# Kernel tuning notes

Hardware: AMD Instinct MI355X
Metric: run time of the kernel (lower is better)

The kernel has to match this reference:

```python
import jax, jax.numpy as jnp
import numpy as np

T, N, DEG = 8, 8192, 15
H = 4


def _gat(x, src, dst, wl, wr, a, b):
    """GATv2Conv with concat=False (heads averaged). x: [N, Cin] -> [N, Cout].
    e_ij = a_h . LeakyReLU(Wl x_j + Wr x_i); softmax over incoming edges of i;
    messages are Wl x_j (PyG GATv2 convention, self-loops already in edge list)."""
    n = x.shape[0]
    h, c = a.shape
    gl = (x @ wl).reshape(n, h, c)  # source-side transform
    gr = (x @ wr).reshape(n, h, c)  # target-side transform
    z = jax.nn.leaky_relu(gl[src] + gr[dst], 0.2)          # [E,H,C]
    e = jnp.einsum('ehc,hc->eh', z, a)                     # [E,H]
    m = jax.ops.segment_max(e, dst, num_segments=n)        # [N,H]
    ex = jnp.exp(e - m[dst])
    den = jax.ops.segment_sum(ex, dst, num_segments=n)     # [N,H]
    msg = jax.ops.segment_sum(ex[:, :, None] * gl[src], dst, num_segments=n)
    return (msg / den[:, :, None]).mean(axis=1) + b


def _d3(x, esrc, edst, wl, wr, a, b):
    # spatio-temporal graph conv: GATv2 applied independently per timestep
    return jax.lax.map(lambda args: _gat(args[0], args[1], args[2], wl, wr, a, b),
                       (x, esrc, edst))


def setup_inputs() -> dict:
    key = jax.random.key(0)
    ks = iter(jax.random.split(key, 32))
    x = jax.random.normal(next(ks), (T, N, 64), dtype=jnp.float32)
    # fixed-degree random graph per timestep + self loops (PyG add_self_loops=True)
    dst_base = jnp.repeat(jnp.arange(N, dtype=jnp.int32), DEG)
    src_r = jax.random.randint(next(ks), (T, N * DEG), 0, N, dtype=jnp.int32)
    loop = jnp.arange(N, dtype=jnp.int32)
    edge_src = jnp.concatenate([src_r, jnp.broadcast_to(loop, (T, N))], axis=1)
    edge_dst = jnp.concatenate([jnp.broadcast_to(dst_base, (T, N * DEG)),
                                jnp.broadcast_to(loop, (T, N))], axis=1)

    def gat_p(k, cin, cout):
        k1, k2, k3 = jax.random.split(k, 3)
        s = 1.0 / np.sqrt(cin)
        return ((jax.random.normal(k1, (cin, H * cout)) * s).astype(jnp.float32),
                (jax.random.normal(k2, (cin, H * cout)) * s).astype(jnp.float32),
                (jax.random.normal(k3, (H, cout)) * s).astype(jnp.float32),
                jnp.zeros((cout,), jnp.float32))

    inp = {"x": x, "edge_src": edge_src, "edge_dst": edge_dst}
    for name, cin, cout in [("c1", 64, 128), ("c2", 128, 64), ("c3", 64, 64), ("c4", 128, 64),
                            ("r11", 64, 64), ("r12", 64, 64), ("r2", 128, 128),
                            ("f11", 64, 64), ("f2", 128, 128)]:
        wl, wr, a, b = gat_p(next(ks), cin, cout)
        inp[name + "_wl"], inp[name + "_wr"], inp[name + "_a"], inp[name + "_b"] = wl, wr, a, b
    # ConvTranspose1d(k=1) == per-node linear conv_ch -> in_channels; then Linear in_channels -> original_dim
    for name, cin, cout in [("r3", 128, 64), ("f3", 128, 64), ("r4", 64, 64), ("f4", 64, 64)]:
        inp[name + "_w"] = (jax.random.normal(next(ks), (cin, cout)) * (1.0 / np.sqrt(cin))).astype(jnp.float32)
        inp[name + "_b"] = jnp.zeros((cout,), jnp.float32)
    return inp


def reference(x, edge_src, edge_dst,
              c1_wl, c1_wr, c1_a, c1_b, c2_wl, c2_wr, c2_a, c2_b,
              c3_wl, c3_wr, c3_a, c3_b, c4_wl, c4_wr, c4_a, c4_b,
              r11_wl, r11_wr, r11_a, r11_b, r12_wl, r12_wr, r12_a, r12_b,
              r2_wl, r2_wr, r2_a, r2_b, r3_w, r3_b, r4_w, r4_b,
              f11_wl, f11_wr, f11_a, f11_b, f2_wl, f2_wr, f2_a, f2_b,
              f3_w, f3_b, f4_w, f4_b):
    elu = jax.nn.elu
    out = elu(_d3(x, edge_src, edge_dst, c1_wl, c1_wr, c1_a, c1_b))           # [T,N,128]
    emb = elu(_d3(out, edge_src, edge_dst, c2_wl, c2_wr, c2_a, c2_b))         # [T,N,64]
    emb = elu(jnp.concatenate([_d3(emb, edge_src, edge_dst, c3_wl, c3_wr, c3_a, c3_b), emb], -1))  # [T,N,128]
    emb = elu(_d3(emb, edge_src, edge_dst, c4_wl, c4_wr, c4_a, c4_b))         # [T,N,64]

    # reconstruction branch on edges at t = -1
    s1, d1 = edge_src[-1], edge_dst[-1]
    r = elu(_gat(emb[-1], s1, d1, r11_wl, r11_wr, r11_a, r11_b))
    r = elu(jnp.concatenate([_gat(r, s1, d1, r12_wl, r12_wr, r12_a, r12_b), r], -1))  # [N,128]
    # F.dropout in eval mode -> identity
    r = elu(_gat(r, s1, d1, r2_wl, r2_wr, r2_a, r2_b))
    r = jnp.tanh(r @ r3_w + r3_b)
    recon = r @ r4_w + r4_b

    # forecasting branch on edges at t = -2 (original reuses reconstruct12 here)
    s2, d2 = edge_src[-2], edge_dst[-2]
    f = elu(_gat(emb[-2], s2, d2, f11_wl, f11_wr, f11_a, f11_b))
    f = elu(jnp.concatenate([_gat(f, s2, d2, r12_wl, r12_wr, r12_a, r12_b), f], -1))
    f = elu(_gat(f, s2, d2, f2_wl, f2_wr, f2_a, f2_b))
    f = jnp.tanh(f @ f3_w + f3_b)
    forecast = f @ f4_w + f4_b
    return (recon, forecast, emb)
```

## Files before the change

### kernel.cpp

```cpp
#include <hip/hip_runtime.h>
#include <cmath>

constexpr int T_   = 8;
constexpr int N_   = 8192;
constexpr int DEG_ = 15;
constexpr int E_   = N_ * (DEG_ + 1);
constexpr float L2E_ = 1.44269504f;

__device__ __forceinline__ float elu1(float v) { return v > 0.f ? v : expm1f(v); }

typedef __attribute__((ext_vector_type(8))) short bf16x8;
typedef __attribute__((ext_vector_type(4))) float f32x4;

__device__ __forceinline__ ushort f2bf(float x) {
  uint u = __float_as_uint(x);
  return (ushort)((u + 0x7FFFu + ((u >> 16) & 1u)) >> 16);
}
__device__ __forceinline__ float bf2f(ushort h) {
  return __uint_as_float(((uint)h) << 16);
}

template<int CTRL>
__device__ __forceinline__ float dpp_add(float x) {
  const int t = __builtin_amdgcn_mov_dpp(__float_as_int(x), CTRL, 0xf, 0xf, true);
  return x + __int_as_float(t);
}
__device__ __forceinline__ float row_reduce16(float x) {
  x = dpp_add<0x121>(x);
  x = dpp_add<0x122>(x);
  x = dpp_add<0x124>(x);
  x = dpp_add<0x128>(x);
  return x;
}

__global__ __launch_bounds__(256) void split_x(
    const float* __restrict__ X, ushort* __restrict__ XH, ushort* __restrict__ XL, int n4)
{
  const int i = blockIdx.x * 256 + threadIdx.x;
  if (i >= n4) return;
  const float4 v = ((const float4*)X)[i];
  const ushort h0 = f2bf(v.x), h1 = f2bf(v.y), h2 = f2bf(v.z), h3 = f2bf(v.w);
  ushort4 hh; hh.x = h0; hh.y = h1; hh.z = h2; hh.w = h3;
  ushort4 ll;
  ll.x = f2bf(v.x - bf2f(h0)); ll.y = f2bf(v.y - bf2f(h1));
  ll.z = f2bf(v.z - bf2f(h2)); ll.w = f2bf(v.w - bf2f(h3));
  ((ushort4*)XH)[i] = hh;
  ((ushort4*)XL)[i] = ll;
}

__global__ __launch_bounds__(256) void split_wt(
    const float* __restrict__ Wl, const float* __restrict__ Wr,
    ushort* __restrict__ WH, ushort* __restrict__ WL, int K, int HC)
{
  const int idx = blockIdx.x * 256 + threadIdx.x;
  if (idx >= 2 * HC * K) return;
  const int k = idx % K;
  const int n = (idx / K) % HC;
  const int s = idx / (K * HC);
  const float v = (s ? Wr : Wl)[k * HC + n];
  const ushort h = f2bf(v);
  WH[idx] = h;
  WL[idx] = f2bf(v - bf2f(h));
}

__global__ __launch_bounds__(256) void gemm_mfma(
    const ushort* __restrict__ Ah, const ushort* __restrict__ Al,
    const ushort* __restrict__ Wh, const ushort* __restrict__ Wl,
    float* __restrict__ Cl, float* __restrict__ Cr,
    int M, int Ncol, int K, int nt)
{
  __shared__ alignas(16) ushort lAh[4 * 1032];
  __shared__ alignas(16) ushort lAl[4 * 1032];
  __shared__ alignas(16) ushort lBh[4 * 520];
  __shared__ alignas(16) ushort lBl[4 * 520];

  const int z = blockIdx.z;
  const int t = (z < nt) ? z : z - nt;
  const int side = (z < nt) ? 0 : 1;
  const ushort* __restrict__ Bh = Wh + (size_t)side * Ncol * K;
  const ushort* __restrict__ Bl = Wl + (size_t)side * Ncol * K;
  float* __restrict__ C = (side ? Cr : Cl) + (size_t)t * M * Ncol;
  const size_t aoff = (size_t)t * M * K;

  const int bm = blockIdx.x * 128, bn = blockIdx.y * 64;
  const int tid = threadIdx.x;
  const int wid = tid >> 6, lane = tid & 63;
  const int l15 = lane & 15, lk = lane >> 4;

  f32x4 acc[2][4] = {};

  for (int k0 = 0; k0 < K; k0 += 32) {
    #pragma unroll
    for (int c = 0; c < 2; c++) {
      const int ch = tid + c * 256;
      const int row = ch >> 2, kc = ch & 3;
      const size_t ga = aoff + (size_t)(bm + row) * K + (k0 + kc * 8);
      *(uint4*)&lAh[kc * 1032 + row * 8] = *(const uint4*)(Ah + ga);
      *(uint4*)&lAl[kc * 1032 + row * 8] = *(const uint4*)(Al + ga);
    }
    {
      const int col = tid >> 2, kc = tid & 3;
      const size_t gb = (size_t)(bn + col) * K + (k0 + kc * 8);
      *(uint4*)&lBh[kc * 520 + col * 8] = *(const uint4*)(Bh + gb);
      *(uint4*)&lBl[kc * 520 + col * 8] = *(const uint4*)(Bl + gb);
    }
    __syncthreads();

    bf16x8 ah[2], al[2], bh4[4], bl4[4];
    const int r0 = wid * 32;
    #pragma unroll
    for (int rf = 0; rf < 2; rf++) {
      const int ro = (r0 + rf * 16 + l15) * 8;
      ah[rf] = *(const bf16x8*)&lAh[lk * 1032 + ro];
      al[rf] = *(const bf16x8*)&lAl[lk * 1032 + ro];
    }
    #pragma unroll
    for (int cf = 0; cf < 4; cf++) {
      const int co = (cf * 16 + l15) * 8;
      bh4[cf] = *(const bf16x8*)&lBh[lk * 520 + co];
      bl4[cf] = *(const bf16x8*)&lBl[lk * 520 + co];
    }
    #pragma unroll
    for (int rf = 0; rf < 2; rf++)
      #pragma unroll
      for (int cf = 0; cf < 4; cf++) {
        acc[rf][cf] = __builtin_amdgcn_mfma_f32_16x16x32_bf16(ah[rf], bh4[cf], acc[rf][cf], 0, 0, 0);
        acc[rf][cf] = __builtin_amdgcn_mfma_f32_16x16x32_bf16(ah[rf], bl4[cf], acc[rf][cf], 0, 0, 0);
        acc[rf][cf] = __builtin_amdgcn_mfma_f32_16x16x32_bf16(al[rf], bh4[cf], acc[rf][cf], 0, 0, 0);
      }
    __syncthreads();
  }

  #pragma unroll
  for (int rf = 0; rf < 2; rf++)
    #pragma unroll
    for (int cf = 0; cf < 4; cf++) {
      const int col = bn + cf * 16 + l15;
      #pragma unroll
      for (int reg = 0; reg < 4; reg++) {
        const int row = bm + wid * 32 + rf * 16 + lk * 4 + reg;
        C[(size_t)row * Ncol + col] = acc[rf][cf][reg];
      }
    }
}

template<int EPI>
__global__ __launch_bounds__(256) void gemm_k(
    const float* __restrict__ A, const float* __restrict__ B,
    float* __restrict__ C, const float* __restrict__ bias,
    int M, int Ncol, int K)
{
  __shared__ float As[16][68];
  __shared__ float Bs[16][64];

  const int tid = threadIdx.x;
  const int tx = tid & 15, ty = tid >> 4;
  const int bm = blockIdx.x * 64, bn = blockIdx.y * 64;

  const int arow = tid >> 2;
  const int akc  = (tid & 3) * 4;
  const int brow = tid >> 4;
  const int bc4  = (tid & 15) * 4;

  float acc[4][4];
  #pragma unroll
  for (int i = 0; i < 4; i++)
    #pragma unroll
    for (int j = 0; j < 4; j++) acc[i][j] = 0.f;

  for (int k0 = 0; k0 < K; k0 += 16) {
    const float4 va = *(const float4*)(A + (size_t)(bm + arow) * K + (k0 + akc));
    const float4 vb = *(const float4*)(B + (size_t)(k0 + brow) * Ncol + (bn + bc4));
    As[akc + 0][arow] = va.x; As[akc + 1][arow] = va.y;
    As[akc + 2][arow] = va.z; As[akc + 3][arow] = va.w;
    *(float4*)&Bs[brow][bc4] = vb;
    __syncthreads();
    #pragma unroll
    for (int kk = 0; kk < 16; kk++) {
      const float4 av = *(const float4*)&As[kk][ty * 4];
      const float4 bv = *(const float4*)&Bs[kk][tx * 4];
      const float a4[4] = {av.x, av.y, av.z, av.w};
      const float b4[4] = {bv.x, bv.y, bv.z, bv.w};
      #pragma unroll
      for (int i = 0; i < 4; i++)
        #pragma unroll
        for (int j = 0; j < 4; j++)
          acc[i][j] = fmaf(a4[i], b4[j], acc[i][j]);
    }
    __syncthreads();
  }

  #pragma unroll
  for (int i = 0; i < 4; i++) {
    const int row = bm + ty * 4 + i;
    const int col = bn + tx * 4;
    float v[4] = {acc[i][0], acc[i][1], acc[i][2], acc[i][3]};
    #pragma unroll
    for (int j = 0; j < 4; j++) v[j] += bias[col + j];
    if (EPI == 1) {
      #pragma unroll
      for (int j = 0; j < 4; j++) v[j] = tanhf(v[j]);
    }
    *(float4*)(C + (size_t)row * Ncol + col) = make_float4(v[0], v[1], v[2], v[3]);
  }
}

template<bool CONCAT>
__global__ __launch_bounds__(256) void gat_agg256(
    const float* __restrict__ GL, const float* __restrict__ GR,
    const float* __restrict__ aw_, const float* __restrict__ bias,
    const int* __restrict__ esrc, float* __restrict__ out,
    const float* __restrict__ csrc,
    ushort* __restrict__ SHo, ushort* __restrict__ SLo, int numNodes)
{
  constexpr int HC = 256, C = 64;
  constexpr int OSTR = CONCAT ? 128 : 64;

  const int lane = threadIdx.x & 63;
  const int wid  = threadIdx.x >> 6;
  const int gid  = blockIdx.x * 4 + wid;
  if (gid >= numNodes) return;
  const int t = gid >> 13;
  const int i = gid & (N_ - 1);

  const float* __restrict__ gl = GL + (size_t)t * N_ * HC;
  const int*   __restrict__ es = esrc + (size_t)t * E_ + (size_t)i * DEG_;

  float gr[4], a6[4], a4c[4];
  {
    const float4 gv = *(const float4*)(GR + (size_t)gid * HC + lane * 4);
    const float4 av = *(const float4*)(aw_ + lane * 4);
    gr[0] = gv.x; gr[1] = gv.y; gr[2] = gv.z; gr[3] = gv.w;
    a6[0] = 0.6f * L2E_ * av.x; a6[1] = 0.6f * L2E_ * av.y;
    a6[2] = 0.6f * L2E_ * av.z; a6[3] = 0.6f * L2E_ * av.w;
    a4c[0] = 0.4f * L2E_ * av.x; a4c[1] = 0.4f * L2E_ * av.y;
    a4c[2] = 0.4f * L2E_ * av.z; a4c[3] = 0.4f * L2E_ * av.w;
  }

  float acc[4] = {0.f, 0.f, 0.f, 0.f};
  float den = 0.f, m = -1e30f;

  #pragma unroll
  for (int b = 0; b < 4; b++) {
    int js[4];
    #pragma unroll
    for (int q = 0; q < 4; q++) {
      const int ek = b * 4 + q;
      js[q] = (ek < DEG_) ? es[ek] : i;
    }
    float g[4][4];
    #pragma unroll
    for (int q = 0; q < 4; q++) {
      const float4 v = *(const float4*)(gl + (size_t)js[q] * HC + lane * 4);
      g[q][0] = v.x; g[q][1] = v.y; g[q][2] = v.z; g[q][3] = v.w;
    }
    float p[4];
    #pragma unroll
    for (int q = 0; q < 4; q++) {
      float s = 0.f;
      #pragma unroll
      for (int u = 0; u < 4; u++) {
        const float z = g[q][u] + gr[u];
        s = fmaf(z, a6[u], s);
        s = fmaf(fabsf(z), a4c[u], s);
      }
      p[q] = s;
    }
    #pragma unroll
    for (int q = 0; q < 4; q++) p[q] = row_reduce16(p[q]);

    const float bmax = fmaxf(fmaxf(p[0], p[1]), fmaxf(p[2], p[3]));
    const float nm   = fmaxf(m, bmax);
    const float sc   = exp2f(m - nm);
    den *= sc;
    #pragma unroll
    for (int u = 0; u < 4; u++) acc[u] *= sc;
    #pragma unroll
    for (int q = 0; q < 4; q++) {
      const float w = exp2f(p[q] - nm);
      den += w;
      #pragma unroll
      for (int u = 0; u < 4; u++) acc[u] = fmaf(w, g[q][u], acc[u]);
    }
    m = nm;
  }

  const float inv = 0.25f / den;
  #pragma unroll
  for (int u = 0; u < 4; u++) acc[u] *= inv;
  #pragma unroll
  for (int u = 0; u < 4; u++) {
    acc[u] += __shfl_xor(acc[u], 16);
    acc[u] += __shfl_xor(acc[u], 32);
  }

  float* orow = out + (size_t)gid * OSTR;
  if (lane < 16) {
    float o[4];
    #pragma unroll
    for (int u = 0; u < 4; u++)
      o[u] = elu1(acc[u] + bias[lane * 4 + u]);
    *(float4*)(orow + lane * 4) = make_float4(o[0], o[1], o[2], o[3]);
    if (SHo) {
      ushort4 hh, ll;
      hh.x = f2bf(o[0]); hh.y = f2bf(o[1]); hh.z = f2bf(o[2]); hh.w = f2bf(o[3]);
      ll.x = f2bf(o[0] - bf2f(hh.x)); ll.y = f2bf(o[1] - bf2f(hh.y));
      ll.z = f2bf(o[2] - bf2f(hh.z)); ll.w = f2bf(o[3] - bf2f(hh.w));
      *(ushort4*)(SHo + (size_t)gid * OSTR + lane * 4) = hh;
      *(ushort4*)(SLo + (size_t)gid * OSTR + lane * 4) = ll;
    }
  } else if (CONCAT && lane < 32) {
    const int q = lane - 16;
    const float4 v = *(const float4*)(csrc + (size_t)gid * C + q * 4);
    const float o0 = elu1(v.x), o1 = elu1(v.y), o2 = elu1(v.z), o3 = elu1(v.w);
    *(float4*)(orow + C + q * 4) = make_float4(o0, o1, o2, o3);
    if (SHo) {
      ushort4 hh, ll;
      hh.x = f2bf(o0); hh.y = f2bf(o1); hh.z = f2bf(o2); hh.w = f2bf(o3);
      ll.x = f2bf(o0 - bf2f(hh.x)); ll.y = f2bf(o1 - bf2f(hh.y));
      ll.z = f2bf(o2 - bf2f(hh.z)); ll.w = f2bf(o3 - bf2f(hh.w));
      *(ushort4*)(SHo + (size_t)gid * OSTR + C + q * 4) = hh;
      *(ushort4*)(SLo + (size_t)gid * OSTR + C + q * 4) = ll;
    }
  }
}

__global__ __launch_bounds__(256) void gat_agg512(
    const float* __restrict__ GL, const float* __restrict__ GR,
    const float* __restrict__ aw_, const float* __restrict__ bias,
    const int* __restrict__ esrc, float* __restrict__ out)
{
  __shared__ float smem[4][128];

  const int lane = threadIdx.x & 63;
  const int h    = threadIdx.x >> 6;
  const int gid  = blockIdx.x;
  const int t = gid >> 13;
  const int i = gid & (N_ - 1);

  const float* __restrict__ gl = GL + (size_t)t * N_ * 512;
  const int*   __restrict__ es = esrc + (size_t)t * E_ + (size_t)i * DEG_;
  const int cb = h * 128 + lane * 2;

  float gr0, gr1, a60, a61, a40, a41;
  {
    const float2 gv = *(const float2*)(GR + (size_t)gid * 512 + cb);
    const float2 av = *(const float2*)(aw_ + cb);
    gr0 = gv.x; gr1 = gv.y;
    a60 = 0.6f * L2E_ * av.x; a61 = 0.6f * L2E_ * av.y;
    a40 = 0.4f * L2E_ * av.x; a41 = 0.4f * L2E_ * av.y;
  }

  float acc0 = 0.f, acc1 = 0.f, den = 0.f, m = -1e30f;

  #pragma unroll
  for (int b = 0; b < 4; b++) {
    int js[4];
    #pragma unroll
    for (int q = 0; q < 4; q++) {
      const int ek = b * 4 + q;
      js[q] = (ek < DEG_) ? es[ek] : i;
    }
    float g[4][2];
    #pragma unroll
    for (int q = 0; q < 4; q++) {
      const float2 v = *(const float2*)(gl + (size_t)js[q] * 512 + cb);
      g[q][0] = v.x; g[q][1] = v.y;
    }
    float p[4];
    #pragma unroll
    for (int q = 0; q < 4; q++) {
      const float z0 = g[q][0] + gr0;
      const float z1 = g[q][1] + gr1;
      float s = z0 * a60;
      s = fmaf(fabsf(z0), a40, s);
      s = fmaf(z1, a61, s);
      s = fmaf(fabsf(z1), a41, s);
      p[q] = s;
    }
    #pragma unroll
    for (int q = 0; q < 4; q++) {
      p[q] = row_reduce16(p[q]);
      p[q] += __shfl_xor(p[q], 16);
      p[q] += __shfl_xor(p[q], 32);
    }
    const float bmax = fmaxf(fmaxf(p[0], p[1]), fmaxf(p[2], p[3]));
    const float nm   = fmaxf(m, bmax);
    const float sc   = exp2f(m - nm);
    den *= sc; acc0 *= sc; acc1 *= sc;
    #pragma unroll
    for (int q = 0; q < 4; q++) {
      const float w = exp2f(p[q] - nm);
      den += w;
      acc0 = fmaf(w, g[q][0], acc0);
      acc1 = fmaf(w, g[q][1], acc1);
    }
    m = nm;
  }

  const float inv = 0.25f / den;
  smem[h][lane * 2]     = acc0 * inv;
  smem[h][lane * 2 + 1] = acc1 * inv;
  __syncthreads();

  if (h == 0) {
    const int c = lane * 2;
    float s0 = smem[0][c] + smem[1][c] + smem[2][c] + smem[3][c];
    float s1 = smem[0][c + 1] + smem[1][c + 1] + smem[2][c + 1] + smem[3][c + 1];
    s0 = elu1(s0 + bias[c]);
    s1 = elu1(s1 + bias[c + 1]);
    *(float2*)(out + (size_t)gid * 128 + c) = make_float2(s0, s1);
  }
}

extern "C" void kernel_launch(void* const* d_in, const int* in_sizes, int n_in,
                              void* d_out, int out_size, void* d_ws, size_t ws_size,
                              hipStream_t stream)
{
  (void)in_sizes; (void)n_in; (void)out_size; (void)ws_size;

  const float* x  = (const float*)d_in[0];
  const int*   es = (const int*)d_in[1];
  const float *c1_wl=(const float*)d_in[3], *c1_wr=(const float*)d_in[4], *c1_a=(const float*)d_in[5], *c1_b=(const float*)d_in[6];
  const float *c2_wl=(const float*)d_in[7], *c2_wr=(const float*)d_in[8], *c2_a=(const float*)d_in[9], *c2_b=(const float*)d_in[10];
  const float *c3_wl=(const float*)d_in[11],*c3_wr=(const float*)d_in[12],*c3_a=(const float*)d_in[13],*c3_b=(const float*)d_in[14];
  const float *c4_wl=(const float*)d_in[15],*c4_wr=(const float*)d_in[16],*c4_a=(const float*)d_in[17],*c4_b=(const float*)d_in[18];
  const float *r11_wl=(const float*)d_in[19],*r11_wr=(const float*)d_in[20],*r11_a=(const float*)d_in[21],*r11_b=(const float*)d_in[22];
  const float *r12_wl=(const float*)d_in[23],*r12_wr=(const float*)d_in[24],*r12_a=(const float*)d_in[25],*r12_b=(const float*)d_in[26];
  const float *r2_wl=(const float*)d_in[27],*r2_wr=(const float*)d_in[28],*r2_a=(const float*)d_in[29],*r2_b=(const float*)d_in[30];
  const float *f11_wl=(const float*)d_in[31],*f11_wr=(const float*)d_in[32],*f11_a=(const float*)d_in[33],*f11_b=(const float*)d_in[34];
  const float *f2_wl=(const float*)d_in[35],*f2_wr=(const float*)d_in[36],*f2_a=(const float*)d_in[37],*f2_b=(const float*)d_in[38];
  const float *r3_w=(const float*)d_in[39], *r3_b=(const float*)d_in[40];
  const float *f3_w=(const float*)d_in[41], *f3_b=(const float*)d_in[42];
  const float *r4_w=(const float*)d_in[43], *r4_b=(const float*)d_in[44];
  const float *f4_w=(const float*)d_in[45], *f4_b=(const float*)d_in[46];

  float* ws = (float*)d_ws;
  float* GL = ws;
  float* GR = GL + (size_t)16777216;
  float* A0 = GR + (size_t)16777216;
  float* A1 = A0 + (size_t)T_ * N_ * 128;
  float* B0 = A1 + (size_t)T_ * N_ * 64;
  float* B1 = B0 + (size_t)N_ * 128;
  ushort* SH = (ushort*)(B1 + (size_t)N_ * 128);
  ushort* SL = SH + (size_t)8388608;
  ushort* WH = SL + (size_t)8388608;
  ushort* WL = WH + (size_t)131072;

  float* recon = (float*)d_out;
  float* fcst  = recon + (size_t)N_ * 64;
  float* emb   = fcst + (size_t)N_ * 64;

  const dim3 blk(256);

  split_x<<<dim3((T_ * N_ * 64 / 4 + 255) / 256), blk, 0, stream>>>(x, SH, SL, T_ * N_ * 64 / 4);
  split_wt<<<dim3((2 * 512 * 64 + 255) / 256), blk, 0, stream>>>(c1_wl, c1_wr, WH, WL, 64, 512);
  for (int ch = 0; ch < 2; ch++) {
    const int t0 = ch * 4, nt = 4;
    gemm_mfma<<<dim3(N_ / 128, 8, 2 * nt), blk, 0, stream>>>(
        SH + (size_t)t0 * N_ * 64, SL + (size_t)t0 * N_ * 64, WH, WL, GL, GR, N_, 512, 64, nt);
    gat_agg512<<<dim3(nt * N_), blk, 0, stream>>>(
        GL, GR, c1_a, c1_b, es + (size_t)t0 * E_, A0 + (size_t)t0 * N_ * 128);
  }
  split_x<<<dim3((T_ * N_ * 128 / 4 + 255) / 256), blk, 0, stream>>>(A0, SH, SL, T_ * N_ * 128 / 4);
  split_wt<<<dim3((2 * 256 * 128 + 255) / 256), blk, 0, stream>>>(c2_wl, c2_wr, WH, WL, 128, 256);
  gemm_mfma<<<dim3(N_ / 128, 4, 2 * T_), blk, 0, stream>>>(SH, SL, WH, WL, GL, GR, N_, 256, 128, T_);
  gat_agg256<false><<<dim3(T_ * N_ / 4), blk, 0, stream>>>(GL, GR, c2_a, c2_b, es, A1, nullptr, SH, SL, T_ * N_);
  split_wt<<<dim3((2 * 256 * 64 + 255) / 256), blk, 0, stream>>>(c3_wl, c3_wr, WH, WL, 64, 256);
  gemm_mfma<<<dim3(N_ / 128, 4, 2 * T_), blk, 0, stream>>>(SH, SL, WH, WL, GL, GR, N_, 256, 64, T_);
  gat_agg256<true><<<dim3(T_ * N_ / 4), blk, 0, stream>>>(GL, GR, c3_a, c3_b, es, A0, A1, SH, SL, T_ * N_);
  split_wt<<<dim3((2 * 256 * 128 + 255) / 256), blk, 0, stream>>>(c4_wl, c4_wr, WH, WL, 128, 256);
  gemm_mfma<<<dim3(N_ / 128, 4, 2 * T_), blk, 0, stream>>>(SH, SL, WH, WL, GL, GR, N_, 256, 128, T_);
  gat_agg256<false><<<dim3(T_ * N_ / 4), blk, 0, stream>>>(GL, GR, c4_a, c4_b, es, emb, nullptr, SH, SL, T_ * N_);

  const int* esR = es + (size_t)7 * E_;
  split_wt<<<dim3((2 * 256 * 64 + 255) / 256), blk, 0, stream>>>(r11_wl, r11_wr, WH, WL, 64, 256);
  gemm_mfma<<<dim3(N_ / 128, 4, 2), blk, 0, stream>>>(SH + (size_t)7 * N_ * 64, SL + (size_t)7 * N_ * 64, WH, WL, GL, GR, N_, 256, 64, 1);
  gat_agg256<false><<<dim3(N_ / 4), blk, 0, stream>>>(GL, GR, r11_a, r11_b, esR, B0, nullptr, SH, SL, N_);
  split_wt<<<dim3((2 * 256 * 64 + 255) / 256), blk, 0, stream>>>(r12_wl, r12_wr, WH, WL, 64, 256);
  gemm_mfma<<<dim3(N_ / 128, 4, 2), blk, 0, stream>>>(SH, SL, WH, WL, GL, GR, N_, 256, 64, 1);
  gat_agg256<true><<<dim3(N_ / 4), blk, 0, stream>>>(GL, GR, r12_a, r12_b, esR, B1, B0, SH, SL, N_);
  split_wt<<<dim3((2 * 512 * 128 + 255) / 256), blk, 0, stream>>>(r2_wl, r2_wr, WH, WL, 128, 512);
  gemm_mfma<<<dim3(N_ / 128, 8, 2), blk, 0, stream>>>(SH, SL, WH, WL, GL, GR, N_, 512, 128, 1);
  gat_agg512<<<dim3(N_), blk, 0, stream>>>(GL, GR, r2_a, r2_b, esR, B0);
  gemm_k<1><<<dim3(N_ / 64, 1, 1), blk, 0, stream>>>(B0, r3_w, B1, r3_b, N_, 64, 128);
  gemm_k<2><<<dim3(N_ / 64, 1, 1), blk, 0, stream>>>(B1, r4_w, recon, r4_b, N_, 64, 64);

  const int* esF = es + (size_t)6 * E_;
  split_wt<<<dim3((2 * 256 * 64 + 255) / 256), blk, 0, stream>>>(f11_wl, f11_wr, WH, WL, 64, 256);
  gemm_mfma<<<dim3(N_ / 128, 4, 2), blk, 0, stream>>>(SH + (size_t)6 * N_ * 64, SL + (size_t)6 * N_ * 64, WH, WL, GL, GR, N_, 256, 64, 1);
  gat_agg256<false><<<dim3(N_ / 4), blk, 0, stream>>>(GL, GR, f11_a, f11_b, esF, B0, nullptr, SH, SL, N_);
  split_wt<<<dim3((2 * 256 * 64 + 255) / 256), blk, 0, stream>>>(r12_wl, r12_wr, WH, WL, 64, 256);
  gemm_mfma<<<dim3(N_ / 128, 4, 2), blk, 0, stream>>>(SH, SL, WH, WL, GL, GR, N_, 256, 64, 1);
  gat_agg256<true><<<dim3(N_ / 4), blk, 0, stream>>>(GL, GR, r12_a, r12_b, esF, B1, B0, SH, SL, N_);
  split_wt<<<dim3((2 * 512 * 128 + 255) / 256), blk, 0, stream>>>(f2_wl, f2_wr, WH, WL, 128, 512);
  gemm_mfma<<<dim3(N_ / 128, 8, 2), blk, 0, stream>>>(SH, SL, WH, WL, GL, GR, N_, 512, 128, 1);
  gat_agg512<<<dim3(N_), blk, 0, stream>>>(GL, GR, f2_a, f2_b, esF, B0);
  gemm_k<1><<<dim3(N_ / 64, 1, 1), blk, 0, stream>>>(B0, f3_w, B1, f3_b, N_, 64, 128);
  gemm_k<2><<<dim3(N_ / 64, 1, 1), blk, 0, stream>>>(B1, f4_w, fcst, f4_b, N_, 64, 64);
}
```

Baseline: 1.036 ms.

## Fuse bf16 hi/lo split into GAT aggregation epilogues and drop unused fp32 writes

```diff
diff --git a/kernel.cpp b/kernel.cpp
--- a/kernel.cpp
+++ b/kernel.cpp
@@ -7,7 +7,9 @@
 constexpr int E_   = N_ * (DEG_ + 1);
 constexpr float L2E_ = 1.44269504f;
 
-__device__ __forceinline__ float elu1(float v) { return v > 0.f ? v : expm1f(v); }
+__device__ __forceinline__ float elu1(float v) {
+  return v > 0.f ? v : exp2f(v * L2E_) - 1.f;
+}
 
 typedef __attribute__((ext_vector_type(8))) short bf16x8;
 typedef __attribute__((ext_vector_type(4))) float f32x4;
@@ -205,7 +207,7 @@
   }
 }
 
-template<bool CONCAT>
+template<bool CONCAT, bool WF32>
 __global__ __launch_bounds__(256) void gat_agg256(
     const float* __restrict__ GL, const float* __restrict__ GR,
     const float* __restrict__ aw_, const float* __restrict__ bias,
@@ -218,13 +220,14 @@
 
   const int lane = threadIdx.x & 63;
   const int wid  = threadIdx.x >> 6;
+  const int t    = blockIdx.x >> 11;
   const int gid  = blockIdx.x * 4 + wid;
   if (gid >= numNodes) return;
-  const int t = gid >> 13;
   const int i = gid & (N_ - 1);
 
   const float* __restrict__ gl = GL + (size_t)t * N_ * HC;
   const int*   __restrict__ es = esrc + (size_t)t * E_ + (size_t)i * DEG_;
+  const uint lo16 = (uint)lane << 4;
 
   float gr[4], a6[4], a4c[4];
   {
@@ -242,16 +245,17 @@
 
   #pragma unroll
   for (int b = 0; b < 4; b++) {
-    int js[4];
+    uint off[4];
     #pragma unroll
     for (int q = 0; q < 4; q++) {
       const int ek = b * 4 + q;
-      js[q] = (ek < DEG_) ? es[ek] : i;
+      const uint j = (uint)((ek < DEG_) ? es[ek] : i);
+      off[q] = (j << 10) + lo16;
     }
     float g[4][4];
     #pragma unroll
     for (int q = 0; q < 4; q++) {
-      const float4 v = *(const float4*)(gl + (size_t)js[q] * HC + lane * 4);
+      const float4 v = *(const float4*)((const char*)gl + off[q]);
       g[q][0] = v.x; g[q][1] = v.y; g[q][2] = v.z; g[q][3] = v.w;
     }
     float p[4];
@@ -294,41 +298,40 @@
     acc[u] += __shfl_xor(acc[u], 32);
   }
 
-  float* orow = out + (size_t)gid * OSTR;
   if (lane < 16) {
     float o[4];
     #pragma unroll
     for (int u = 0; u < 4; u++)
       o[u] = elu1(acc[u] + bias[lane * 4 + u]);
-    *(float4*)(orow + lane * 4) = make_float4(o[0], o[1], o[2], o[3]);
-    if (SHo) {
-      ushort4 hh, ll;
-      hh.x = f2bf(o[0]); hh.y = f2bf(o[1]); hh.z = f2bf(o[2]); hh.w = f2bf(o[3]);
-      ll.x = f2bf(o[0] - bf2f(hh.x)); ll.y = f2bf(o[1] - bf2f(hh.y));
-      ll.z = f2bf(o[2] - bf2f(hh.z)); ll.w = f2bf(o[3] - bf2f(hh.w));
-      *(ushort4*)(SHo + (size_t)gid * OSTR + lane * 4) = hh;
-      *(ushort4*)(SLo + (size_t)gid * OSTR + lane * 4) = ll;
-    }
+    if (WF32)
+      *(float4*)(out + (size_t)gid * OSTR + lane * 4) = make_float4(o[0], o[1], o[2], o[3]);
+    ushort4 hh, ll;
+    hh.x = f2bf(o[0]); hh.y = f2bf(o[1]); hh.z = f2bf(o[2]); hh.w = f2bf(o[3]);
+    ll.x = f2bf(o[0] - bf2f(hh.x)); ll.y = f2bf(o[1] - bf2f(hh.y));
+    ll.z = f2bf(o[2] - bf2f(hh.z)); ll.w = f2bf(o[3] - bf2f(hh.w));
+    *(ushort4*)(SHo + (size_t)gid * OSTR + lane * 4) = hh;
+    *(ushort4*)(SLo + (size_t)gid * OSTR + lane * 4) = ll;
   } else if (CONCAT && lane < 32) {
     const int q = lane - 16;
     const float4 v = *(const float4*)(csrc + (size_t)gid * C + q * 4);
     const float o0 = elu1(v.x), o1 = elu1(v.y), o2 = elu1(v.z), o3 = elu1(v.w);
-    *(float4*)(orow + C + q * 4) = make_float4(o0, o1, o2, o3);
-    if (SHo) {
-      ushort4 hh, ll;
-      hh.x = f2bf(o0); hh.y = f2bf(o1); hh.z = f2bf(o2); hh.w = f2bf(o3);
-      ll.x = f2bf(o0 - bf2f(hh.x)); ll.y = f2bf(o1 - bf2f(hh.y));
-      ll.z = f2bf(o2 - bf2f(hh.z)); ll.w = f2bf(o3 - bf2f(hh.w));
-      *(ushort4*)(SHo + (size_t)gid * OSTR + C + q * 4) = hh;
-      *(ushort4*)(SLo + (size_t)gid * OSTR + C + q * 4) = ll;
-    }
-  }
-}
-
+    if (WF32)
+      *(float4*)(out + (size_t)gid * OSTR + C + q * 4) = make_float4(o0, o1, o2, o3);
+    ushort4 hh, ll;
+    hh.x = f2bf(o0); hh.y = f2bf(o1); hh.z = f2bf(o2); hh.w = f2bf(o3);
+    ll.x = f2bf(o0 - bf2f(hh.x)); ll.y = f2bf(o1 - bf2f(hh.y));
+    ll.z = f2bf(o2 - bf2f(hh.z)); ll.w = f2bf(o3 - bf2f(hh.w));
+    *(ushort4*)(SHo + (size_t)gid * OSTR + C + q * 4) = hh;
+    *(ushort4*)(SLo + (size_t)gid * OSTR + C + q * 4) = ll;
+  }
+}
+
+template<bool WF32, bool SPLIT>
 __global__ __launch_bounds__(256) void gat_agg512(
     const float* __restrict__ GL, const float* __restrict__ GR,
     const float* __restrict__ aw_, const float* __restrict__ bias,
-    const int* __restrict__ esrc, float* __restrict__ out)
+    const int* __restrict__ esrc, float* __restrict__ out,
+    ushort* __restrict__ SHo, ushort* __restrict__ SLo)
 {
   __shared__ float smem[4][128];
 
@@ -341,6 +344,7 @@
   const float* __restrict__ gl = GL + (size_t)t * N_ * 512;
   const int*   __restrict__ es = esrc + (size_t)t * E_ + (size_t)i * DEG_;
   const int cb = h * 128 + lane * 2;
+  const uint cbo = (uint)cb << 2;
 
   float gr0, gr1, a60, a61, a40, a41;
   {
@@ -355,16 +359,17 @@
 
   #pragma unroll
   for (int b = 0; b < 4; b++) {
-    int js[4];
+    uint off[4];
     #pragma unroll
     for (int q = 0; q < 4; q++) {
       const int ek = b * 4 + q;
-      js[q] = (ek < DEG_) ? es[ek] : i;
+      const uint j = (uint)((ek < DEG_) ? es[ek] : i);
+      off[q] = (j << 11) + cbo;
     }
     float g[4][2];
     #pragma unroll
     for (int q = 0; q < 4; q++) {
-      const float2 v = *(const float2*)(gl + (size_t)js[q] * 512 + cb);
+      const float2 v = *(const float2*)((const char*)gl + off[q]);
       g[q][0] = v.x; g[q][1] = v.y;
     }
     float p[4];
@@ -409,7 +414,15 @@
     float s1 = smem[0][c + 1] + smem[1][c + 1] + smem[2][c + 1] + smem[3][c + 1];
     s0 = elu1(s0 + bias[c]);
     s1 = elu1(s1 + bias[c + 1]);
-    *(float2*)(out + (size_t)gid * 128 + c) = make_float2(s0, s1);
+    if (WF32)
+      *(float2*)(out + (size_t)gid * 128 + c) = make_float2(s0, s1);
+    if (SPLIT) {
+      ushort2 hh, ll;
+      hh.x = f2bf(s0); hh.y = f2bf(s1);
+      ll.x = f2bf(s0 - bf2f(hh.x)); ll.y = f2bf(s1 - bf2f(hh.y));
+      *(ushort2*)(SHo + (size_t)gid * 128 + c) = hh;
+      *(ushort2*)(SLo + (size_t)gid * 128 + c) = ll;
+    }
   }
 }
 
@@ -438,14 +451,15 @@
   float* ws = (float*)d_ws;
   float* GL = ws;
   float* GR = GL + (size_t)16777216;
-  float* A0 = GR + (size_t)16777216;
-  float* A1 = A0 + (size_t)T_ * N_ * 128;
+  float* A1 = GR + (size_t)16777216;
   float* B0 = A1 + (size_t)T_ * N_ * 64;
   float* B1 = B0 + (size_t)N_ * 128;
-  ushort* SH = (ushort*)(B1 + (size_t)N_ * 128);
-  ushort* SL = SH + (size_t)8388608;
-  ushort* WH = SL + (size_t)8388608;
-  ushort* WL = WH + (size_t)131072;
+  ushort* SH  = (ushort*)(B1 + (size_t)N_ * 128);
+  ushort* SL  = SH + (size_t)8388608;
+  ushort* SH2 = SL + (size_t)8388608;
+  ushort* SL2 = SH2 + (size_t)8388608;
+  ushort* WH  = SL2 + (size_t)8388608;
+  ushort* WL  = WH + (size_t)131072;
 
   float* recon = (float*)d_out;
   float* fcst  = recon + (size_t)N_ * 64;
@@ -453,49 +467,58 @@
 
   const dim3 blk(256);
 
-  split_x<<<dim3((T_ * N_ * 64 / 4 + 255) / 256), blk, 0, stream>>>(x, SH, SL, T_ * N_ * 64 / 4);
+  split_x<<<dim3(T_ * N_ * 64 / 4 / 256), blk, 0, stream>>>(x, SH, SL, T_ * N_ * 64 / 4);
   split_wt<<<dim3((2 * 512 * 64 + 255) / 256), blk, 0, stream>>>(c1_wl, c1_wr, WH, WL, 64, 512);
   for (int ch = 0; ch < 2; ch++) {
     const int t0 = ch * 4, nt = 4;
     gemm_mfma<<<dim3(N_ / 128, 8, 2 * nt), blk, 0, stream>>>(
         SH + (size_t)t0 * N_ * 64, SL + (size_t)t0 * N_ * 64, WH, WL, GL, GR, N_, 512, 64, nt);
-    gat_agg512<<<dim3(nt * N_), blk, 0, stream>>>(
-        GL, GR, c1_a, c1_b, es + (size_t)t0 * E_, A0 + (size_t)t0 * N_ * 128);
-  }
-  split_x<<<dim3((T_ * N_ * 128 / 4 + 255) / 256), blk, 0, stream>>>(A0, SH, SL, T_ * N_ * 128 / 4);
+    gat_agg512<false, true><<<dim3(nt * N_), blk, 0, stream>>>(
+        GL, GR, c1_a, c1_b, es + (size_t)t0 * E_, nullptr,
+        SH2 + (size_t)t0 * N_ * 128, SL2 + (size_t)t0 * N_ * 128);
+  }
   split_wt<<<dim3((2 * 256 * 128 + 255) / 256), blk, 0, stream>>>(c2_wl, c2_wr, WH, WL, 128, 256);
-  gemm_mfma<<<dim3(N_ / 128, 4, 2 * T_), blk, 0, stream>>>(SH, SL, WH, WL, GL, GR, N_, 256, 128, T_);
-  gat_agg256<false><<<dim3(T_ * N_ / 4), blk, 0, stream>>>(GL, GR, c2_a, c2_b, es, A1, nullptr, SH, SL, T_ * N_);
+  gemm_mfma<<<dim3(N_ / 128, 4, 2 * T_), blk, 0, stream>>>(SH2, SL2, WH, WL, GL, GR, N_, 256, 128, T_);
+  gat_agg256<false, true><<<dim3(T_ * N_ / 4), blk, 0, stream>>>(
+      GL, GR, c2_a, c2_b, es, A1, nullptr, SH, SL, T_ * N_);
   split_wt<<<dim3((2 * 256 * 64 + 255) / 256), blk, 0, stream>>>(c3_wl, c3_wr, WH, WL, 64, 256);
   gemm_mfma<<<dim3(N_ / 128, 4, 2 * T_), blk, 0, stream>>>(SH, SL, WH, WL, GL, GR, N_, 256, 64, T_);
-  gat_agg256<true><<<dim3(T_ * N_ / 4), blk, 0, stream>>>(GL, GR, c3_a, c3_b, es, A0, A1, SH, SL, T_ * N_);
+  gat_agg256<true, false><<<dim3(T_ * N_ / 4), blk, 0, stream>>>(
+      GL, GR, c3_a, c3_b, es, nullptr, A1, SH, SL, T_ * N_);
   split_wt<<<dim3((2 * 256 * 128 + 255) / 256), blk, 0, stream>>>(c4_wl, c4_wr, WH, WL, 128, 256);
   gemm_mfma<<<dim3(N_ / 128, 4, 2 * T_), blk, 0, stream>>>(SH, SL, WH, WL, GL, GR, N_, 256, 128, T_);
-  gat_agg256<false><<<dim3(T_ * N_ / 4), blk, 0, stream>>>(GL, GR, c4_a, c4_b, es, emb, nullptr, SH, SL, T_ * N_);
+  gat_agg256<false, true><<<dim3(T_ * N_ / 4), blk, 0, stream>>>(
+      GL, GR, c4_a, c4_b, es, emb, nullptr, SH2, SL2, T_ * N_);
 
   const int* esR = es + (size_t)7 * E_;
   split_wt<<<dim3((2 * 256 * 64 + 255) / 256), blk, 0, stream>>>(r11_wl, r11_wr, WH, WL, 64, 256);
-  gemm_mfma<<<dim3(N_ / 128, 4, 2), blk, 0, stream>>>(SH + (size_t)7 * N_ * 64, SL + (size_t)7 * N_ * 64, WH, WL, GL, GR, N_, 256, 64, 1);
-  gat_agg256<false><<<dim3(N_ / 4), blk, 0, stream>>>(GL, GR, r11_a, r11_b, esR, B0, nullptr, SH, SL, N_);
+  gemm_mfma<<<dim3(N_ / 128, 4, 2), blk, 0, stream>>>(
+      SH2 + (size_t)7 * N_ * 64, SL2 + (size_t)7 * N_ * 64, WH, WL, GL, GR, N_, 256, 64, 1);
+  gat_agg256<false, true><<<dim3(N_ / 4), blk, 0, stream>>>(
+      GL, GR, r11_a, r11_b, esR, B0, nullptr, SH, SL, N_);
   split_wt<<<dim3((2 * 256 * 64 + 255) / 256), blk, 0, stream>>>(r12_wl, r12_wr, WH, WL, 64, 256);
   gemm_mfma<<<dim3(N_ / 128, 4, 2), blk, 0, stream>>>(SH, SL, WH, WL, GL, GR, N_, 256, 64, 1);
-  gat_agg256<true><<<dim3(N_ / 4), blk, 0, stream>>>(GL, GR, r12_a, r12_b, esR, B1, B0, SH, SL, N_);
+  gat_agg256<true, false><<<dim3(N_ / 4), blk, 0, stream>>>(
+      GL, GR, r12_a, r12_b, esR, nullptr, B0, SH, SL, N_);
   split_wt<<<dim3((2 * 512 * 128 + 255) / 256), blk, 0, stream>>>(r2_wl, r2_wr, WH, WL, 128, 512);
   gemm_mfma<<<dim3(N_ / 128, 8, 2), blk, 0, stream>>>(SH, SL, WH, WL, GL, GR, N_, 512, 128, 1);
-  gat_agg512<<<dim3(N_), blk, 0, stream>>>(GL, GR, r2_a, r2_b, esR, B0);
+  gat_agg512<true, false><<<dim3(N_), blk, 0, stream>>>(GL, GR, r2_a, r2_b, esR, B0, nullptr, nullptr);
   gemm_k<1><<<dim3(N_ / 64, 1, 1), blk, 0, stream>>>(B0, r3_w, B1, r3_b, N_, 64, 128);
   gemm_k<2><<<dim3(N_ / 64, 1, 1), blk, 0, stream>>>(B1, r4_w, recon, r4_b, N_, 64, 64);
 
   const int* esF = es + (size_t)6 * E_;
   split_wt<<<dim3((2 * 256 * 64 + 255) / 256), blk, 0, stream>>>(f11_wl, f11_wr, WH, WL, 64, 256);
-  gemm_mfma<<<dim3(N_ / 128, 4, 2), blk, 0, stream>>>(SH + (size_t)6 * N_ * 64, SL + (size_t)6 * N_ * 64, WH, WL, GL, GR, N_, 256, 64, 1);
-  gat_agg256<false><<<dim3(N_ / 4), blk, 0, stream>>>(GL, GR, f11_a, f11_b, esF, B0, nullptr, SH, SL, N_);
+  gemm_mfma<<<dim3(N_ / 128, 4, 2), blk, 0, stream>>>(
+      SH2 + (size_t)6 * N_ * 64, SL2 + (size_t)6 * N_ * 64, WH, WL, GL, GR, N_, 256, 64, 1);
+  gat_agg256<false, true><<<dim3(N_ / 4), blk, 0, stream>>>(
+      GL, GR, f11_a, f11_b, esF, B0, nullptr, SH, SL, N_);
   split_wt<<<dim3((2 * 256 * 64 + 255) / 256), blk, 0, stream>>>(r12_wl, r12_wr, WH, WL, 64, 256);
   gemm_mfma<<<dim3(N_ / 128, 4, 2), blk, 0, stream>>>(SH, SL, WH, WL, GL, GR, N_, 256, 64, 1);
-  gat_agg256<true><<<dim3(N_ / 4), blk, 0, stream>>>(GL, GR, r12_a, r12_b, esF, B1, B0, SH, SL, N_);
+  gat_agg256<true, false><<<dim3(N_ / 4), blk, 0, stream>>>(
+      GL, GR, r12_a, r12_b, esF, nullptr, B0, SH, SL, N_);
   split_wt<<<dim3((2 * 512 * 128 + 255) / 256), blk, 0, stream>>>(f2_wl, f2_wr, WH, WL, 128, 512);
   gemm_mfma<<<dim3(N_ / 128, 8, 2), blk, 0, stream>>>(SH, SL, WH, WL, GL, GR, N_, 512, 128, 1);
-  gat_agg512<<<dim3(N_), blk, 0, stream>>>(GL, GR, f2_a, f2_b, esF, B0);
+  gat_agg512<true, false><<<dim3(N_), blk, 0, stream>>>(GL, GR, f2_a, f2_b, esF, B0, nullptr, nullptr);
   gemm_k<1><<<dim3(N_ / 64, 1, 1), blk, 0, stream>>>(B0, f3_w, B1, f3_b, N_, 64, 128);
   gemm_k<2><<<dim3(N_ / 64, 1, 1), blk, 0, stream>>>(B1, f4_w, fcst, f4_b, N_, 64, 64);
 }
```

Result: faster. 1.011 ms (-2.4%).
